# Kernel optimization log

Measured on AMD Instinct MI355X. Metric: run time of the kernel, lower is better.

The kernel has to match this reference:

```python
import jax, jax.numpy as jnp
import numpy as np

N = 100000      # nodes
E = 1600000     # edges
IN, H, OUT = 128, 128, 64
P_DROP = 0.5


def _glorot_linear(key, out_d, in_d):
    # PyG Linear default init (kaiming-uniform-ish); exact init is irrelevant for the baseline
    bound = 1.0 / np.sqrt(in_d)
    return jax.random.uniform(key, (out_d, in_d), jnp.float32, -bound, bound)


def setup_inputs() -> dict:
    key = jax.random.key(0)
    ks = jax.random.split(key, 8)
    x = jax.random.normal(ks[0], (N, IN), jnp.float32)
    edge_index = jax.random.randint(ks[1], (2, E), 0, N, dtype=jnp.int64)
    W1l = _glorot_linear(ks[2], H, IN)
    b1 = jnp.zeros((H,), jnp.float32)
    W1r = _glorot_linear(ks[3], H, IN)
    W2l = _glorot_linear(ks[4], OUT, H)
    b2 = jnp.zeros((OUT,), jnp.float32)
    W2r = _glorot_linear(ks[5], OUT, H)
    return dict(x=x, edge_index=edge_index, W1l=W1l, b1=b1, W1r=W1r,
                W2l=W2l, b2=b2, W2r=W2r)


def _sage_conv(x, src, dst, Wl, bl, Wr):
    # PyG SAGEConv (aggr='mean'): out = lin_l(mean_{j in N(i)} x_j) + lin_r(x_i)
    msg = x[src]                                             # [E, d] gather
    agg = jax.ops.segment_sum(msg, dst, num_segments=N)      # [N, d] scatter-add
    cnt = jax.ops.segment_sum(jnp.ones((src.shape[0], 1), x.dtype), dst,
                              num_segments=N)                # [N, 1] in-degree
    mean = agg / jnp.maximum(cnt, 1.0)                       # isolated nodes -> 0
    return mean @ Wl.T + bl + x @ Wr.T


def reference(x, edge_index, W1l, b1, W1r, W2l, b2, W2r):
    src, dst = edge_index[0], edge_index[1]
    h = _sage_conv(x, src, dst, W1l, b1, W1r)
    h = jax.nn.relu(h)
    # F.dropout(p=0.5) made deterministic with a fixed key
    keep = jax.random.bernoulli(jax.random.key(42), 1.0 - P_DROP, h.shape)
    h = jnp.where(keep, h / (1.0 - P_DROP), 0.0)
    return _sage_conv(h, src, dst, W2l, b2, W2r)
```

## Files before the change

### kernel.cpp

```cpp
#include <hip/hip_runtime.h>
#include <hip/hip_bf16.h>

#define N_NODES 100000
#define NE      1600000

#define BINSH 7
#define NBIN  782
#define BCAP  3072
#define SEPB  16384
#define NBLK  ((NE + SEPB - 1) / SEPB)
#define NMASKW 200000

typedef __attribute__((ext_vector_type(8))) short bfrag;
typedef __attribute__((ext_vector_type(4))) float ffrag;

#define BFLO(u) __uint_as_float((u) << 16)
#define BFHI(u) __uint_as_float((u) & 0xffff0000u)

__device__ __forceinline__ unsigned tf_rotl(unsigned x, int d) {
    return (x << d) | (x >> (32 - d));
}

__device__ __forceinline__ unsigned tf_word(unsigned f) {
    const unsigned ks0 = 0u;
    const unsigned ks1 = 42u;
    const unsigned ks2 = 0x1BD11BDAu ^ 0u ^ 42u;
    unsigned x0 = 0u + ks0;
    unsigned x1 = f + ks1;
#define TF_RND(r) { x0 += x1; x1 = tf_rotl(x1, r); x1 ^= x0; }
    TF_RND(13) TF_RND(15) TF_RND(26) TF_RND(6)
    x0 += ks1; x1 += ks2 + 1u;
    TF_RND(17) TF_RND(29) TF_RND(16) TF_RND(24)
    x0 += ks2; x1 += ks0 + 2u;
    TF_RND(13) TF_RND(15) TF_RND(26) TF_RND(6)
    x0 += ks0; x1 += ks1 + 3u;
    TF_RND(17) TF_RND(29) TF_RND(16) TF_RND(24)
    x0 += ks1; x1 += ks2 + 4u;
    TF_RND(13) TF_RND(15) TF_RND(26) TF_RND(6)
    x0 += ks2; x1 += ks0 + 5u;
#undef TF_RND
    return x0 ^ x1;
}

__device__ __forceinline__ unsigned short bf_bits(float v) {
    __hip_bfloat16 b = __float2bfloat16(v);
    return *(unsigned short*)&b;
}

__global__ void k_mask(unsigned long long* __restrict__ km) {
    const int lane = threadIdx.x & 63;
    const int w0 = (blockIdx.x * blockDim.x + threadIdx.x) >> 6;
    const int nw = (gridDim.x * blockDim.x) >> 6;
    for (int widx = w0; widx < NMASKW; widx += nw) {
        unsigned wv = tf_word((unsigned)widx * 64u + (unsigned)lane);
        unsigned long long keep = __ballot(!(wv & 0x80000000u));
        if (lane == 0) km[widx] = keep;
    }
}

__global__ void k_detect(const int* __restrict__ ei, int* __restrict__ flag,
                         int* __restrict__ bincur) {
    __shared__ int nz;
    if (threadIdx.x == 0) nz = 0;
    __syncthreads();
    for (int i = threadIdx.x; i < 1024; i += blockDim.x) {
        if (ei[2 * i + 1] != 0) atomicAdd(&nz, 1);
        bincur[i] = 0;
    }
    __syncthreads();
    if (threadIdx.x == 0) *flag = (nz == 0) ? 1 : 0;
}

__global__ void k_conv(const float4* __restrict__ in, ushort4* __restrict__ out,
                       int n4) {
    int i = blockIdx.x * blockDim.x + threadIdx.x;
    if (i < n4) {
        float4 v = in[i];
        ushort4 o;
        o.x = bf_bits(v.x);
        o.y = bf_bits(v.y);
        o.z = bf_bits(v.z);
        o.w = bf_bits(v.w);
        out[i] = o;
    }
}

__global__ void k_wconv(const float* __restrict__ a, const float* __restrict__ b,
                        const float* __restrict__ c, const float* __restrict__ d,
                        __hip_bfloat16* __restrict__ o) {
    int i = blockIdx.x * blockDim.x + threadIdx.x;
    if (i < 16384)      o[i] = __float2bfloat16(a[i]);
    else if (i < 32768) o[i] = __float2bfloat16(b[i - 16384]);
    else if (i < 40960) o[i] = __float2bfloat16(c[i - 32768]);
    else if (i < 49152) o[i] = __float2bfloat16(d[i - 40960]);
}

__global__ __launch_bounds__(1024) void k_binscatter(const int* __restrict__ ei,
        const int* __restrict__ flag, int* __restrict__ bincur,
        int* __restrict__ pairs) {
    __shared__ int h[NBIN];
    __shared__ int lbase[NBIN];
    for (int i = threadIdx.x; i < NBIN; i += 1024) h[i] = 0;
    __syncthreads();
    const int is64 = *flag;
    const int e0 = blockIdx.x * SEPB + threadIdx.x;
    int d[16], s[16];
#pragma unroll
    for (int k = 0; k < 16; ++k) {
        int e = e0 + k * 1024;
        if (e < NE) {
            d[k] = is64 ? ei[2 * (NE + e)] : ei[NE + e];
            s[k] = is64 ? ei[2 * e]        : ei[e];
            atomicAdd(&h[d[k] >> BINSH], 1);
        } else {
            d[k] = -1; s[k] = 0;
        }
    }
    __syncthreads();
    for (int i = threadIdx.x; i < NBIN; i += 1024) {
        int c = h[i];
        lbase[i] = c ? atomicAdd(&bincur[i], c) : 0;
        h[i] = 0;
    }
    __syncthreads();
#pragma unroll
    for (int k = 0; k < 16; ++k) {
        if (d[k] >= 0) {
            int b = d[k] >> BINSH;
            int r = atomicAdd(&h[b], 1);
            pairs[(size_t)b * BCAP + lbase[b] + r] =
                ((d[k] & 127) << 17) | s[k];
        }
    }
}

__global__ __launch_bounds__(256) void k_bin2csr(const int* __restrict__ pairs,
        const int* __restrict__ bincnt, int* __restrict__ ptr,
        int* __restrict__ adj) {
    __shared__ int red[256];
    __shared__ int cnt[128];
    __shared__ int sc[128];
    __shared__ int woff[128];
    const int b = blockIdx.x;
    const int t = threadIdx.x;
    int s = 0;
    for (int i = t; i < b; i += 256) s += bincnt[i];
    red[t] = s;
    __syncthreads();
    for (int o = 128; o > 0; o >>= 1) {
        if (t < o) red[t] += red[t + o];
        __syncthreads();
    }
    const int base = red[0];
    const int nb = bincnt[b];
    const int* pb = pairs + (size_t)b * BCAP;
    if (t < 128) cnt[t] = 0;
    __syncthreads();
    for (int i = t; i < nb; i += 256)
        atomicAdd(&cnt[(pb[i] >> 17) & 127], 1);
    __syncthreads();
    if (t < 128) sc[t] = cnt[t];
    __syncthreads();
    for (int o = 1; o < 128; o <<= 1) {
        int u = 0;
        if (t < 128 && t >= o) u = sc[t - o];
        __syncthreads();
        if (t < 128) sc[t] += u;
        __syncthreads();
    }
    if (t < 128) {
        int ex = sc[t] - cnt[t];
        int node = b * 128 + t;
        if (node <= N_NODES) ptr[node] = base + ex;
        woff[t] = ex;
    }
    __syncthreads();
    for (int i = t; i < nb; i += 256) {
        int pk = pb[i];
        int r = atomicAdd(&woff[(pk >> 17) & 127], 1);
        adj[base + r] = pk & 0x1FFFF;
    }
}

__global__ void k_agg(const __hip_bfloat16* __restrict__ feat,
                      const int* __restrict__ ptr, const int* __restrict__ adj,
                      __hip_bfloat16* __restrict__ mean) {
    const int wid = (blockIdx.x * blockDim.x + threadIdx.x) >> 6;
    const int lane = threadIdx.x & 63;
    if (wid >= N_NODES) return;
    const int p0 = ptr[wid], p1 = ptr[wid + 1];
    const int half = lane >> 5;
    const size_t coff = (size_t)(lane & 31) * 4;
    float c0 = 0.f, c1 = 0.f, c2 = 0.f, c3 = 0.f;
    float d0 = 0.f, d1 = 0.f, d2 = 0.f, d3 = 0.f;
    int p = p0;
    for (; p + 15 < p1; p += 16) {
        int s[8];
#pragma unroll
        for (int k = 0; k < 8; ++k) s[k] = adj[p + 2 * k + half];
#pragma unroll
        for (int k = 0; k < 8; ++k) {
            uint2 u = *(const uint2*)(feat + (size_t)s[k] * 128 + coff);
            if (k & 1) { d0 += BFLO(u.x); d1 += BFHI(u.x); d2 += BFLO(u.y); d3 += BFHI(u.y); }
            else       { c0 += BFLO(u.x); c1 += BFHI(u.x); c2 += BFLO(u.y); c3 += BFHI(u.y); }
        }
    }
    for (; p + 7 < p1; p += 8) {
        int s[4];
#pragma unroll
        for (int k = 0; k < 4; ++k) s[k] = adj[p + 2 * k + half];
#pragma unroll
        for (int k = 0; k < 4; ++k) {
            uint2 u = *(const uint2*)(feat + (size_t)s[k] * 128 + coff);
            if (k & 1) { d0 += BFLO(u.x); d1 += BFHI(u.x); d2 += BFLO(u.y); d3 += BFHI(u.y); }
            else       { c0 += BFLO(u.x); c1 += BFHI(u.x); c2 += BFLO(u.y); c3 += BFHI(u.y); }
        }
    }
    for (; p + 1 < p1; p += 2) {
        int s = adj[p + half];
        uint2 u = *(const uint2*)(feat + (size_t)s * 128 + coff);
        c0 += BFLO(u.x); c1 += BFHI(u.x); c2 += BFLO(u.y); c3 += BFHI(u.y);
    }
    if (p < p1 && half == 0) {
        int s = adj[p];
        uint2 u = *(const uint2*)(feat + (size_t)s * 128 + coff);
        c0 += BFLO(u.x); c1 += BFHI(u.x); c2 += BFLO(u.y); c3 += BFHI(u.y);
    }
    c0 += d0; c1 += d1; c2 += d2; c3 += d3;
    c0 += __shfl_xor(c0, 32);
    c1 += __shfl_xor(c1, 32);
    c2 += __shfl_xor(c2, 32);
    c3 += __shfl_xor(c3, 32);
    if (half == 0) {
        const float inv = 1.0f / (float)max(p1 - p0, 1);
        uint2 o;
        o.x = ((unsigned)bf_bits(c1 * inv) << 16) | (unsigned)bf_bits(c0 * inv);
        o.y = ((unsigned)bf_bits(c3 * inv) << 16) | (unsigned)bf_bits(c2 * inv);
        *(uint2*)(mean + (size_t)wid * 128 + coff) = o;
    }
}

__global__ __launch_bounds__(256) void k_lin1f(
    const __hip_bfloat16* __restrict__ Am, const __hip_bfloat16* __restrict__ Ax,
    const __hip_bfloat16* __restrict__ W1l, const __hip_bfloat16* __restrict__ W1r,
    const float* __restrict__ b1,
    const __hip_bfloat16* __restrict__ W2l, const __hip_bfloat16* __restrict__ W2r,
    const float* __restrict__ b2,
    const unsigned long long* __restrict__ kmask,
    __hip_bfloat16* __restrict__ y2, float* __restrict__ zout) {
    __shared__ __align__(16) __hip_bfloat16 hs[64][136];
    const int tid = threadIdx.x;
    const int w  = tid >> 6;
    const int l  = tid & 63;
    const int lr = l & 15;
    const int lk = l >> 4;
    const int j0 = w * 32;
    const int j2 = w * 16 + lr;
    const int n0 = blockIdx.x * 64;

    bfrag B1[2][2][4];
#pragma unroll
    for (int jt = 0; jt < 2; ++jt) {
        const int jrow = j0 + jt * 16 + lr;
#pragma unroll
        for (int ks = 0; ks < 4; ++ks) {
            B1[jt][0][ks] = *(const bfrag*)(W1l + jrow * 128 + ks * 32 + lk * 8);
            B1[jt][1][ks] = *(const bfrag*)(W1r + jrow * 128 + ks * 32 + lk * 8);
        }
    }
    bfrag Bl2[4], Br2[4];
#pragma unroll
    for (int ks = 0; ks < 4; ++ks) {
        Bl2[ks] = *(const bfrag*)(W2l + j2 * 128 + ks * 32 + lk * 8);
        Br2[ks] = *(const bfrag*)(W2r + j2 * 128 + ks * 32 + lk * 8);
    }
    const float bj0 = b1[j0 + lr];
    const float bj1 = b1[j0 + 16 + lr];
    const float bj2 = b2[j2];

    for (int t = 0; t < 4; ++t) {
        const int rbase = n0 + t * 16;
        int arow = rbase + lr;
        if (arow > N_NODES - 1) arow = N_NODES - 1;
        ffrag acc0 = {0.f, 0.f, 0.f, 0.f};
        ffrag acc1 = {0.f, 0.f, 0.f, 0.f};
#pragma unroll
        for (int ks = 0; ks < 4; ++ks) {
            bfrag am = *(const bfrag*)(Am + (size_t)arow * 128 + ks * 32 + lk * 8);
            bfrag ax = *(const bfrag*)(Ax + (size_t)arow * 128 + ks * 32 + lk * 8);
            acc0 = __builtin_amdgcn_mfma_f32_16x16x32_bf16(am, B1[0][0][ks], acc0, 0, 0, 0);
            acc1 = __builtin_amdgcn_mfma_f32_16x16x32_bf16(am, B1[1][0][ks], acc1, 0, 0, 0);
            acc0 = __builtin_amdgcn_mfma_f32_16x16x32_bf16(ax, B1[0][1][ks], acc0, 0, 0, 0);
            acc1 = __builtin_amdgcn_mfma_f32_16x16x32_bf16(ax, B1[1][1][ks], acc1, 0, 0, 0);
        }
#pragma unroll
        for (int r = 0; r < 4; ++r) {
            const int n = rbase + lk * 4 + r;
            const int lrow = t * 16 + lk * 4 + r;
            const int nm = (n < N_NODES) ? n : (N_NODES - 1);
            const unsigned long long km = kmask[nm * 2 + (j0 >> 6)];
            float v0 = fmaxf(acc0[r] + bj0, 0.f);
            v0 = ((km >> ((j0 + lr) & 63)) & 1ull) ? (v0 + v0) : 0.f;
            hs[lrow][j0 + lr] = __float2bfloat16(v0);
            float v1 = fmaxf(acc1[r] + bj1, 0.f);
            v1 = ((km >> ((j0 + 16 + lr) & 63)) & 1ull) ? (v1 + v1) : 0.f;
            hs[lrow][j0 + 16 + lr] = __float2bfloat16(v1);
        }
    }
    __syncthreads();

    for (int t = 0; t < 4; ++t) {
        ffrag accY = {0.f, 0.f, 0.f, 0.f};
        ffrag accZ = {0.f, 0.f, 0.f, 0.f};
#pragma unroll
        for (int ks = 0; ks < 4; ++ks) {
            bfrag ah = *(const bfrag*)&hs[t * 16 + lr][ks * 32 + lk * 8];
            accY = __builtin_amdgcn_mfma_f32_16x16x32_bf16(ah, Bl2[ks], accY, 0, 0, 0);
            accZ = __builtin_amdgcn_mfma_f32_16x16x32_bf16(ah, Br2[ks], accZ, 0, 0, 0);
        }
#pragma unroll
        for (int r = 0; r < 4; ++r) {
            const int n = n0 + t * 16 + lk * 4 + r;
            if (n < N_NODES) {
                y2[(size_t)n * 64 + j2]   = __float2bfloat16(accY[r]);
                zout[(size_t)n * 64 + j2] = accZ[r] + bj2;
            }
        }
    }
}

__global__ void k_agg2f(const __hip_bfloat16* __restrict__ feat,
                        const int* __restrict__ ptr, const int* __restrict__ adj,
                        float* __restrict__ out) {
    const int node = (blockIdx.x * blockDim.x + threadIdx.x) >> 5;
    const int sl = threadIdx.x & 31;
    if (node >= N_NODES) return;
    const int p0 = ptr[node], p1 = ptr[node + 1];
    const int sub = sl >> 4;
    const size_t coff = (size_t)(sl & 15) * 4;
    float c0 = 0.f, c1 = 0.f, c2 = 0.f, c3 = 0.f;
    float d0 = 0.f, d1 = 0.f, d2 = 0.f, d3 = 0.f;
    int p = p0;
    for (; p + 15 < p1; p += 16) {
        int s[8];
#pragma unroll
        for (int k = 0; k < 8; ++k) s[k] = adj[p + 2 * k + sub];
#pragma unroll
        for (int k = 0; k < 8; ++k) {
            uint2 u = *(const uint2*)(feat + (size_t)s[k] * 64 + coff);
            if (k & 1) { d0 += BFLO(u.x); d1 += BFHI(u.x); d2 += BFLO(u.y); d3 += BFHI(u.y); }
            else       { c0 += BFLO(u.x); c1 += BFHI(u.x); c2 += BFLO(u.y); c3 += BFHI(u.y); }
        }
    }
    for (; p + 7 < p1; p += 8) {
        int s[4];
#pragma unroll
        for (int k = 0; k < 4; ++k) s[k] = adj[p + 2 * k + sub];
#pragma unroll
        for (int k = 0; k < 4; ++k) {
            uint2 u = *(const uint2*)(feat + (size_t)s[k] * 64 + coff);
            if (k & 1) { d0 += BFLO(u.x); d1 += BFHI(u.x); d2 += BFLO(u.y); d3 += BFHI(u.y); }
            else       { c0 += BFLO(u.x); c1 += BFHI(u.x); c2 += BFLO(u.y); c3 += BFHI(u.y); }
        }
    }
    for (; p + 1 < p1; p += 2) {
        int s = adj[p + sub];
        uint2 u = *(const uint2*)(feat + (size_t)s * 64 + coff);
        c0 += BFLO(u.x); c1 += BFHI(u.x); c2 += BFLO(u.y); c3 += BFHI(u.y);
    }
    if (p < p1 && sub == 0) {
        int s = adj[p];
        uint2 u = *(const uint2*)(feat + (size_t)s * 64 + coff);
        c0 += BFLO(u.x); c1 += BFHI(u.x); c2 += BFLO(u.y); c3 += BFHI(u.y);
    }
    c0 += d0; c1 += d1; c2 += d2; c3 += d3;
    c0 += __shfl_xor(c0, 16);
    c1 += __shfl_xor(c1, 16);
    c2 += __shfl_xor(c2, 16);
    c3 += __shfl_xor(c3, 16);
    if (sub == 0) {
        const float inv = 1.0f / (float)max(p1 - p0, 1);
        float4 z = *(const float4*)(out + (size_t)node * 64 + coff);
        z.x += c0 * inv;
        z.y += c1 * inv;
        z.z += c2 * inv;
        z.w += c3 * inv;
        *(float4*)(out + (size_t)node * 64 + coff) = z;
    }
}

extern "C" void kernel_launch(void* const* d_in, const int* in_sizes, int n_in,
                              void* d_out, int out_size, void* d_ws, size_t ws_size,
                              hipStream_t stream) {
    const float* x   = (const float*)d_in[0];
    const int*   ei  = (const int*)d_in[1];
    const float* W1l = (const float*)d_in[2];
    const float* b1  = (const float*)d_in[3];
    const float* W1r = (const float*)d_in[4];
    const float* W2l = (const float*)d_in[5];
    const float* b2  = (const float*)d_in[6];
    const float* W2r = (const float*)d_in[7];
    float* out = (float*)d_out;

    char* w = (char*)d_ws;
    int* flag   = (int*)w;
    int* bincur = flag + 64;
    int* ptr    = bincur + 1024;
    int* adj    = ptr + (N_NODES + 1);
    size_t koff = (((size_t)(64 + 1024 + N_NODES + 1 + NE)) * 4 + 255)
                  & ~(size_t)255;
    unsigned long long* kmask = (unsigned long long*)(w + koff);
    size_t foff = (koff + (size_t)NMASKW * 8 + 255) & ~(size_t)255;
    __hip_bfloat16* wb    = (__hip_bfloat16*)(w + foff);
    __hip_bfloat16* w1lb  = wb;
    __hip_bfloat16* w1rb  = wb + 16384;
    __hip_bfloat16* w2lb  = wb + 32768;
    __hip_bfloat16* w2rb  = wb + 40960;
    __hip_bfloat16* xb    = wb + 49152;
    __hip_bfloat16* meanb = xb + (size_t)N_NODES * 128;
    char* pregion = (char*)(meanb + (size_t)N_NODES * 128);
    int* pairs = (int*)pregion;
    __hip_bfloat16* y2b = (__hip_bfloat16*)pregion;

    const int n4 = N_NODES * 128 / 4;
    k_conv<<<(n4 + 255) / 256, 256, 0, stream>>>((const float4*)x, (ushort4*)xb, n4);
    k_wconv<<<192, 256, 0, stream>>>(W1l, W1r, W2l, W2r, wb);
    k_detect<<<1, 256, 0, stream>>>(ei, flag, bincur);
    k_mask<<<1024, 256, 0, stream>>>(kmask);

    k_binscatter<<<NBLK, 1024, 0, stream>>>(ei, flag, bincur, pairs);
    k_bin2csr<<<NBIN, 256, 0, stream>>>(pairs, bincur, ptr, adj);

    const int ab  = (N_NODES + 3) / 4;
    const int nb  = (N_NODES + 63) / 64;
    const int ab2 = (N_NODES + 7) / 8;

    k_agg<<<ab, 256, 0, stream>>>(xb, ptr, adj, meanb);
    k_lin1f<<<nb, 256, 0, stream>>>(meanb, xb, w1lb, w1rb, b1,
                                    w2lb, w2rb, b2, kmask, y2b, out);
    k_agg2f<<<ab2, 256, 0, stream>>>(y2b, ptr, adj, out);
}
```

Baseline: 243.2 us.

## Fuse preprocessing kernels and halve lin1f row tile with prefetched A fragments

Merges the four preprocessing launches (x conversion, weight conversion, int64 detection, dropout mask) into one grid-stride kernel to cut launch overhead. Separately, k_lin1f now processes 32 rows per block instead of 64, doubling the block count. It also software-prefetches the next 16-row A fragments into registers while the current ones feed MFMA. Bounds checks are dropped because N is divisible by 32, which adds register pressure and relies on that exact size.

```diff
diff --git a/kernel.cpp b/kernel.cpp
--- a/kernel.cpp
+++ b/kernel.cpp
@@ -47,52 +47,50 @@
     return *(unsigned short*)&b;
 }
 
-__global__ void k_mask(unsigned long long* __restrict__ km) {
+__global__ __launch_bounds__(256) void k_pre(
+    const float4* __restrict__ x4, ushort4* __restrict__ xb4,
+    const float* __restrict__ W1l, const float* __restrict__ W1r,
+    const float* __restrict__ W2l, const float* __restrict__ W2r,
+    __hip_bfloat16* __restrict__ wb,
+    const int* __restrict__ ei, int* __restrict__ flag,
+    int* __restrict__ bincur, unsigned long long* __restrict__ km) {
+    const int tid0 = blockIdx.x * 256 + threadIdx.x;
+    const int stride = gridDim.x * 256;
+
+    for (int i = tid0; i < N_NODES * 128 / 4; i += stride) {
+        float4 v = x4[i];
+        ushort4 o;
+        o.x = bf_bits(v.x); o.y = bf_bits(v.y);
+        o.z = bf_bits(v.z); o.w = bf_bits(v.w);
+        xb4[i] = o;
+    }
+    for (int i = tid0; i < 49152; i += stride) {
+        float v;
+        if (i < 16384)      v = W1l[i];
+        else if (i < 32768) v = W1r[i - 16384];
+        else if (i < 40960) v = W2l[i - 32768];
+        else                v = W2r[i - 40960];
+        wb[i] = __float2bfloat16(v);
+    }
+    if (blockIdx.x == 0) {
+        __shared__ int nz;
+        if (threadIdx.x == 0) nz = 0;
+        __syncthreads();
+        for (int i = threadIdx.x; i < 1024; i += 256) {
+            if (ei[2 * i + 1] != 0) atomicAdd(&nz, 1);
+            bincur[i] = 0;
+        }
+        __syncthreads();
+        if (threadIdx.x == 0) *flag = (nz == 0) ? 1 : 0;
+    }
     const int lane = threadIdx.x & 63;
-    const int w0 = (blockIdx.x * blockDim.x + threadIdx.x) >> 6;
-    const int nw = (gridDim.x * blockDim.x) >> 6;
-    for (int widx = w0; widx < NMASKW; widx += nw) {
+    const int gw = tid0 >> 6;
+    const int nw = stride >> 6;
+    for (int widx = gw; widx < NMASKW; widx += nw) {
         unsigned wv = tf_word((unsigned)widx * 64u + (unsigned)lane);
         unsigned long long keep = __ballot(!(wv & 0x80000000u));
         if (lane == 0) km[widx] = keep;
     }
-}
-
-__global__ void k_detect(const int* __restrict__ ei, int* __restrict__ flag,
-                         int* __restrict__ bincur) {
-    __shared__ int nz;
-    if (threadIdx.x == 0) nz = 0;
-    __syncthreads();
-    for (int i = threadIdx.x; i < 1024; i += blockDim.x) {
-        if (ei[2 * i + 1] != 0) atomicAdd(&nz, 1);
-        bincur[i] = 0;
-    }
-    __syncthreads();
-    if (threadIdx.x == 0) *flag = (nz == 0) ? 1 : 0;
-}
-
-__global__ void k_conv(const float4* __restrict__ in, ushort4* __restrict__ out,
-                       int n4) {
-    int i = blockIdx.x * blockDim.x + threadIdx.x;
-    if (i < n4) {
-        float4 v = in[i];
-        ushort4 o;
-        o.x = bf_bits(v.x);
-        o.y = bf_bits(v.y);
-        o.z = bf_bits(v.z);
-        o.w = bf_bits(v.w);
-        out[i] = o;
-    }
-}
-
-__global__ void k_wconv(const float* __restrict__ a, const float* __restrict__ b,
-                        const float* __restrict__ c, const float* __restrict__ d,
-                        __hip_bfloat16* __restrict__ o) {
-    int i = blockIdx.x * blockDim.x + threadIdx.x;
-    if (i < 16384)      o[i] = __float2bfloat16(a[i]);
-    else if (i < 32768) o[i] = __float2bfloat16(b[i - 16384]);
-    else if (i < 40960) o[i] = __float2bfloat16(c[i - 32768]);
-    else if (i < 49152) o[i] = __float2bfloat16(d[i - 40960]);
 }
 
 __global__ __launch_bounds__(1024) void k_binscatter(const int* __restrict__ ei,
@@ -248,7 +246,7 @@
     const float* __restrict__ b2,
     const unsigned long long* __restrict__ kmask,
     __hip_bfloat16* __restrict__ y2, float* __restrict__ zout) {
-    __shared__ __align__(16) __hip_bfloat16 hs[64][136];
+    __shared__ __align__(16) __hip_bfloat16 hs[32][136];
     const int tid = threadIdx.x;
     const int w  = tid >> 6;
     const int l  = tid & 63;
@@ -256,7 +254,7 @@
     const int lk = l >> 4;
     const int j0 = w * 32;
     const int j2 = w * 16 + lr;
-    const int n0 = blockIdx.x * 64;
+    const int n0 = blockIdx.x * 32;
 
     bfrag B1[2][2][4];
 #pragma unroll
@@ -278,27 +276,39 @@
     const float bj1 = b1[j0 + 16 + lr];
     const float bj2 = b2[j2];
 
-    for (int t = 0; t < 4; ++t) {
-        const int rbase = n0 + t * 16;
-        int arow = rbase + lr;
-        if (arow > N_NODES - 1) arow = N_NODES - 1;
+    bfrag amc[4], axc[4], amn[4], axn[4];
+    {
+        const size_t arow = (size_t)(n0 + lr);
+#pragma unroll
+        for (int ks = 0; ks < 4; ++ks) {
+            amc[ks] = *(const bfrag*)(Am + arow * 128 + ks * 32 + lk * 8);
+            axc[ks] = *(const bfrag*)(Ax + arow * 128 + ks * 32 + lk * 8);
+        }
+    }
+#pragma unroll
+    for (int t = 0; t < 2; ++t) {
+        if (t < 1) {
+            const size_t arow = (size_t)(n0 + 16 + lr);
+#pragma unroll
+            for (int ks = 0; ks < 4; ++ks) {
+                amn[ks] = *(const bfrag*)(Am + arow * 128 + ks * 32 + lk * 8);
+                axn[ks] = *(const bfrag*)(Ax + arow * 128 + ks * 32 + lk * 8);
+            }
+        }
         ffrag acc0 = {0.f, 0.f, 0.f, 0.f};
         ffrag acc1 = {0.f, 0.f, 0.f, 0.f};
 #pragma unroll
         for (int ks = 0; ks < 4; ++ks) {
-            bfrag am = *(const bfrag*)(Am + (size_t)arow * 128 + ks * 32 + lk * 8);
-            bfrag ax = *(const bfrag*)(Ax + (size_t)arow * 128 + ks * 32 + lk * 8);
-            acc0 = __builtin_amdgcn_mfma_f32_16x16x32_bf16(am, B1[0][0][ks], acc0, 0, 0, 0);
-            acc1 = __builtin_amdgcn_mfma_f32_16x16x32_bf16(am, B1[1][0][ks], acc1, 0, 0, 0);
-            acc0 = __builtin_amdgcn_mfma_f32_16x16x32_bf16(ax, B1[0][1][ks], acc0, 0, 0, 0);
-            acc1 = __builtin_amdgcn_mfma_f32_16x16x32_bf16(ax, B1[1][1][ks], acc1, 0, 0, 0);
+            acc0 = __builtin_amdgcn_mfma_f32_16x16x32_bf16(amc[ks], B1[0][0][ks], acc0, 0, 0, 0);
+            acc1 = __builtin_amdgcn_mfma_f32_16x16x32_bf16(amc[ks], B1[1][0][ks], acc1, 0, 0, 0);
+            acc0 = __builtin_amdgcn_mfma_f32_16x16x32_bf16(axc[ks], B1[0][1][ks], acc0, 0, 0, 0);
+            acc1 = __builtin_amdgcn_mfma_f32_16x16x32_bf16(axc[ks], B1[1][1][ks], acc1, 0, 0, 0);
         }
 #pragma unroll
         for (int r = 0; r < 4; ++r) {
-            const int n = rbase + lk * 4 + r;
+            const int n = n0 + t * 16 + lk * 4 + r;
             const int lrow = t * 16 + lk * 4 + r;
-            const int nm = (n < N_NODES) ? n : (N_NODES - 1);
-            const unsigned long long km = kmask[nm * 2 + (j0 >> 6)];
+            const unsigned long long km = kmask[n * 2 + (j0 >> 6)];
             float v0 = fmaxf(acc0[r] + bj0, 0.f);
             v0 = ((km >> ((j0 + lr) & 63)) & 1ull) ? (v0 + v0) : 0.f;
             hs[lrow][j0 + lr] = __float2bfloat16(v0);
@@ -306,10 +316,13 @@
             v1 = ((km >> ((j0 + 16 + lr) & 63)) & 1ull) ? (v1 + v1) : 0.f;
             hs[lrow][j0 + 16 + lr] = __float2bfloat16(v1);
         }
-    }
-    __syncthreads();
-
-    for (int t = 0; t < 4; ++t) {
+#pragma unroll
+        for (int ks = 0; ks < 4; ++ks) { amc[ks] = amn[ks]; axc[ks] = axn[ks]; }
+    }
+    __syncthreads();
+
+#pragma unroll
+    for (int t = 0; t < 2; ++t) {
         ffrag accY = {0.f, 0.f, 0.f, 0.f};
         ffrag accZ = {0.f, 0.f, 0.f, 0.f};
 #pragma unroll
@@ -321,10 +334,8 @@
 #pragma unroll
         for (int r = 0; r < 4; ++r) {
             const int n = n0 + t * 16 + lk * 4 + r;
-            if (n < N_NODES) {
-                y2[(size_t)n * 64 + j2]   = __float2bfloat16(accY[r]);
-                zout[(size_t)n * 64 + j2] = accZ[r] + bj2;
-            }
+            y2[(size_t)n * 64 + j2]   = __float2bfloat16(accY[r]);
+            zout[(size_t)n * 64 + j2] = accZ[r] + bj2;
         }
     }
 }
@@ -422,21 +433,19 @@
     int* pairs = (int*)pregion;
     __hip_bfloat16* y2b = (__hip_bfloat16*)pregion;
 
-    const int n4 = N_NODES * 128 / 4;
-    k_conv<<<(n4 + 255) / 256, 256, 0, stream>>>((const float4*)x, (ushort4*)xb, n4);
-    k_wconv<<<192, 256, 0, stream>>>(W1l, W1r, W2l, W2r, wb);
-    k_detect<<<1, 256, 0, stream>>>(ei, flag, bincur);
-    k_mask<<<1024, 256, 0, stream>>>(kmask);
+    k_pre<<<2048, 256, 0, stream>>>((const float4*)x, (ushort4*)xb,
+                                    W1l, W1r, W2l, W2r, wb,
+                                    ei, flag, bincur, kmask);
 
     k_binscatter<<<NBLK, 1024, 0, stream>>>(ei, flag, bincur, pairs);
     k_bin2csr<<<NBIN, 256, 0, stream>>>(pairs, bincur, ptr, adj);
 
     const int ab  = (N_NODES + 3) / 4;
-    const int nb  = (N_NODES + 63) / 64;
+    const int nb1 = N_NODES / 32;
     const int ab2 = (N_NODES + 7) / 8;
 
     k_agg<<<ab, 256, 0, stream>>>(xb, ptr, adj, meanb);
-    k_lin1f<<<nb, 256, 0, stream>>>(meanb, xb, w1lb, w1rb, b1,
-                                    w2lb, w2rb, b2, kmask, y2b, out);
+    k_lin1f<<<nb1, 256, 0, stream>>>(meanb, xb, w1lb, w1rb, b1,
+                                     w2lb, w2rb, b2, kmask, y2b, out);
     k_agg2f<<<ab2, 256, 0, stream>>>(y2b, ptr, adj, out);
 }
```

After: 243.2 us. Within noise of the previous version (-0.0%).
